# Optimization experiments

Hardware: AMD Instinct MI355X
Metric: run time of the kernel (lower is better)

Reference implementation:

```python
import jax, jax.numpy as jnp
import numpy as np

STATE_DIM, ACTION_DIM, HIDDEN_DIM = 512, 64, 2048
INPUT_DIM = STATE_DIM + ACTION_DIM + 1  # 577
BATCH = 4096


def setup_inputs() -> dict:
    key = jax.random.key(0)
    ks = jax.random.split(key, 12)
    sc_x = 1.0 / np.sqrt(INPUT_DIM)
    sc_h = 1.0 / np.sqrt(HIDDEN_DIM)
    return {
        "s": jax.random.normal(ks[0], (BATCH, STATE_DIM), jnp.float32),
        "a_prev": jax.random.normal(ks[1], (BATCH, ACTION_DIM), jnp.float32),
        "r_prev": jax.random.normal(ks[2], (BATCH, 1), jnp.float32),
        "h": jnp.zeros((HIDDEN_DIM,), jnp.float32),
        "c": jnp.zeros((HIDDEN_DIM,), jnp.float32),
        # Fused gate weights: columns ordered [i, f, g(c-tilde), o]
        "Wx": jax.random.uniform(ks[3], (INPUT_DIM, 4 * HIDDEN_DIM), jnp.float32, -sc_x, sc_x),
        "Wh": jax.random.uniform(ks[4], (HIDDEN_DIM, 4 * HIDDEN_DIM), jnp.float32, -sc_h, sc_h),
        "bh": jax.random.uniform(ks[5], (4 * HIDDEN_DIM,), jnp.float32, -sc_h, sc_h),
        "Wa": jax.random.uniform(ks[6], (HIDDEN_DIM, ACTION_DIM), jnp.float32, -sc_h, sc_h),
        "ba": jax.random.uniform(ks[7], (ACTION_DIM,), jnp.float32, -sc_h, sc_h),
        "Wv": jax.random.uniform(ks[8], (HIDDEN_DIM, 1), jnp.float32, -sc_h, sc_h),
        "bv": jax.random.uniform(ks[9], (1,), jnp.float32, -sc_h, sc_h),
    }


def reference(s, a_prev, r_prev, h, c, Wx, Wh, bh, Wa, ba, Wv, bv):
    # x: [B, input_dim]
    x = jnp.concatenate([s, a_prev, r_prev], axis=1)
    # Two fused GEMMs replace the 8 separate small linears (same math).
    z = x @ Wx + h @ Wh + bh          # [B, 4H]
    zi, zf, zg, zo = jnp.split(z, 4, axis=-1)
    i = jax.nn.sigmoid(zi)
    f = jax.nn.sigmoid(zf)
    c_new = f * c + i * jnp.tanh(zg)  # [B, H] (c broadcast over batch)
    o = jax.nn.sigmoid(zo)
    h_new = o * jnp.tanh(c_new)       # [B, H]
    probs = jax.nn.softmax(h_new @ Wa + ba, axis=1)  # [B, A]
    v = h_new @ Wv + bv               # [B, 1]
    return (probs, v)
```

## Files before the change

kernel.cpp:

```cpp
#include <hip/hip_runtime.h>
#include <hip/hip_bf16.h>

#define BATCH   4096
#define SDIM    512
#define ADIM    64
#define IDIM    577
#define KP2     640
#define NKT     20
#define HDIM    2048
#define ZDIM    8192
#define BUFE    (128 * 32)

typedef __attribute__((ext_vector_type(8))) __bf16 bf16x8;
typedef __attribute__((ext_vector_type(4))) float  accx4;

__global__ __launch_bounds__(256) void setup_kernel(
    const float* __restrict__ s, const float* __restrict__ a_prev,
    const float* __restrict__ r_prev, const float* __restrict__ h,
    const float* __restrict__ wx, const float* __restrict__ wh,
    const float* __restrict__ wa,
    __hip_bfloat16* __restrict__ xb, __hip_bfloat16* __restrict__ wxt,
    __hip_bfloat16* __restrict__ waT, float* __restrict__ zh_w)
{
    __shared__ float stile[64 * 65];
    const int bid = blockIdx.x;
    const int t = threadIdx.x;

    if (bid < 1280) {
        const int kt2 = bid >> 7;
        const int nt  = bid & 127;
        const int c4  = t & 15;
        const int rr  = t >> 4;
#pragma unroll
        for (int i = 0; i < 4; ++i) {
            const int r = rr + i * 16;
            const int k = kt2 * 64 + r;
            float4 v = (k < IDIM)
                ? *(const float4*)(wx + (size_t)k * ZDIM + nt * 64 + c4 * 4)
                : float4{0.f, 0.f, 0.f, 0.f};
            *(float4*)(stile + r * 65 + c4 * 4) = v;
        }
        __syncthreads();
        const int ch = t & 7;
#pragma unroll
        for (int i = 0; i < 2; ++i) {
            const int nr = (t >> 3) + i * 32;
            bf16x8 w8;
#pragma unroll
            for (int j = 0; j < 8; ++j)
                w8[j] = (__bf16)stile[(ch * 8 + j) * 65 + nr];
            *(bf16x8*)(wxt + (size_t)(nt * 64 + nr) * KP2 + kt2 * 64 + ch * 8)
                = w8;
        }
    } else if (bid < 1536) {
        const int zb = bid - 1280;
        const int nb = zb & 31, ky = zb >> 5;
        const int n  = nb * 256 + t;
        const float* hp  = h + ky * 256;
        const float* whp = wh + (size_t)ky * 256 * ZDIM + n;
        float p = 0.0f;
#pragma unroll 16
        for (int kk = 0; kk < 256; ++kk)
            p = fmaf(hp[kk], whp[(size_t)kk * ZDIM], p);
        zh_w[ky * ZDIM + n] = p;
    } else if (bid < 5632) {
        const int row = bid - 1536;
        const float* srow = s + (size_t)row * SDIM;
        const float* arow = a_prev + (size_t)row * ADIM;
        __hip_bfloat16* xrow = xb + (size_t)row * KP2;
        for (int c = t; c < KP2; c += 256) {
            float v;
            if (c < SDIM)        v = srow[c];
            else if (c < 576)    v = arow[c - SDIM];
            else if (c == 576)   v = r_prev[row];
            else                 v = 0.0f;
            xrow[c] = __float2bfloat16(v);
        }
    } else {
        const int wb = bid - 5632;
        const int kt = wb >> 1, at = wb & 1;
        const int c  = t & 31, r0 = t >> 5;
#pragma unroll
        for (int i = 0; i < 4; ++i) {
            int r = r0 + i * 8;
            stile[r * 33 + c] = wa[(size_t)(kt * 32 + r) * ADIM + at * 32 + c];
        }
        __syncthreads();
#pragma unroll
        for (int i = 0; i < 4; ++i) {
            int r = r0 + i * 8;
            waT[(size_t)(at * 32 + r) * HDIM + kt * 32 + c] =
                __float2bfloat16(stile[c * 33 + r]);
        }
    }
}

__global__ __launch_bounds__(256) void zh_reduce(
    const float* __restrict__ zh_w, const float* __restrict__ bh,
    float* __restrict__ zh)
{
    const int j = blockIdx.x * 256 + threadIdx.x;
    float v = bh[j];
#pragma unroll
    for (int p = 0; p < 8; ++p)
        v += zh_w[p * ZDIM + j];
    zh[j] = v;
}

__device__ __forceinline__ float sigmoid_f(float x) {
    return 1.0f / (1.0f + __expf(-x));
}
__device__ __forceinline__ float tanh_f(float x) {
    return 1.0f - 2.0f / (1.0f + __expf(2.0f * x));
}

__global__ __launch_bounds__(256, 3) void lstm_gemm(
    const __hip_bfloat16* __restrict__ xb,
    const __hip_bfloat16* __restrict__ wxt,
    const float* __restrict__ zh,
    const float* __restrict__ cvec,
    __hip_bfloat16* __restrict__ hout)
{
    __shared__ __bf16 smA[2 * BUFE];
    __shared__ __bf16 smB[2 * BUFE];
    const int t    = threadIdx.x;
    const int lane = t & 63;
    const int wid  = t >> 6;
    const int m0   = blockIdx.x * 128;
    const int n0   = blockIdx.y * 32;
    const int wm   = wid >> 1, wn = wid & 1;
    const int fl15 = lane & 15;
    const int fhi  = lane >> 4;

    accx4 acc[4][4] = {};

    const int cch = (lane & 3) ^ ((lane >> 2) & 3) ^ ((lane >> 4) & 3);
    const __bf16* gA[2]; const __bf16* gB[2]; int lofs[2];
#pragma unroll
    for (int i = 0; i < 2; ++i) {
        const int rbase = wid * 32 + i * 16;
        const int r = rbase + (lane >> 2);
        gA[i] = (const __bf16*)xb + (size_t)(m0 + r) * KP2 + cch * 8;
        const int g = r >> 5, nn = r & 31;
        gB[i] = (const __bf16*)wxt +
                (size_t)(g * HDIM + n0 + nn) * KP2 + cch * 8;
        lofs[i] = rbase * 32;
    }

    auto stage = [&](int tile, int p) {
        const int ko = tile * 32;
        const int po = p * BUFE;
#pragma unroll
        for (int i = 0; i < 2; ++i) {
            __builtin_amdgcn_global_load_lds(
                (const __attribute__((address_space(1))) void*)(gA[i] + ko),
                (__attribute__((address_space(3))) void*)(smA + po + lofs[i]),
                16, 0, 0);
            __builtin_amdgcn_global_load_lds(
                (const __attribute__((address_space(1))) void*)(gB[i] + ko),
                (__attribute__((address_space(3))) void*)(smB + po + lofs[i]),
                16, 0, 0);
        }
    };

    const int sl = ((fhi ^ (fl15 & 3) ^ ((fl15 >> 2) & 3)) * 8);

    auto compute = [&](int p) {
        const int po = p * BUFE;
        bf16x8 af[4], bfr[4];
#pragma unroll
        for (int rt = 0; rt < 4; ++rt)
            af[rt] = *(const bf16x8*)(smA + po +
                (wm * 64 + rt * 16 + fl15) * 32 + sl);
#pragma unroll
        for (int g = 0; g < 4; ++g)
            bfr[g] = *(const bf16x8*)(smB + po +
                (g * 32 + wn * 16 + fl15) * 32 + sl);
#pragma unroll
        for (int g = 0; g < 4; ++g)
#pragma unroll
            for (int rt = 0; rt < 4; ++rt)
                acc[g][rt] = __builtin_amdgcn_mfma_f32_16x16x32_bf16(
                    af[rt], bfr[g], acc[g][rt], 0, 0, 0);
    };

    stage(0, 0);
    __syncthreads();
#pragma unroll
    for (int kt = 0; kt < NKT - 1; ++kt) {
        stage(kt + 1, (kt + 1) & 1);
        compute(kt & 1);
        __syncthreads();
    }
    compute((NKT - 1) & 1);

    const int colg = n0 + wn * 16 + fl15;
    const float zhi = zh[colg];
    const float zhf = zh[HDIM + colg];
    const float zhg = zh[2 * HDIM + colg];
    const float zho = zh[3 * HDIM + colg];
    const float cv  = cvec[colg];
#pragma unroll
    for (int rt = 0; rt < 4; ++rt) {
#pragma unroll
        for (int r = 0; r < 4; ++r) {
            const int row = m0 + wm * 64 + rt * 16 + (fhi << 2) + r;
            const float zi = acc[0][rt][r] + zhi;
            const float zf = acc[1][rt][r] + zhf;
            const float zg = acc[2][rt][r] + zhg;
            const float zo = acc[3][rt][r] + zho;
            const float cn = sigmoid_f(zf) * cv + sigmoid_f(zi) * tanh_f(zg);
            const float hn = sigmoid_f(zo) * tanh_f(cn);
            hout[(size_t)row * HDIM + colg] = __float2bfloat16(hn);
        }
    }
}

__global__ __launch_bounds__(512) void head_kernel(
    const __hip_bfloat16* __restrict__ hnew,
    const __hip_bfloat16* __restrict__ waT,
    const float* __restrict__ wv,
    const float* __restrict__ ba, const float* __restrict__ bv,
    float* __restrict__ probs, float* __restrict__ vout)
{
    __shared__ float lg[2][16][68];
    __shared__ float vpart[2][16];
    const int t    = threadIdx.x;
    const int lane = t & 63;
    const int wid  = t >> 6;
    const int kh   = wid >> 2;
    const int wid2 = wid & 3;
    const int r0   = blockIdx.x * 16;
    const int fl15 = lane & 15, fhi = lane >> 4;

    const __bf16* arow = (const __bf16*)hnew +
        (size_t)(r0 + fl15) * HDIM + kh * 1024 + fhi * 8;
    const __bf16* brow = (const __bf16*)waT +
        (size_t)(wid2 * 16 + fl15) * HDIM + kh * 1024 + fhi * 8;
    const float* wvp = wv + kh * 1024 + fhi * 8;
    const bool do_v = (wid2 == 0);

    accx4 acc0 = {}, acc1 = {};
    float va0 = 0.f, va1 = 0.f, va2 = 0.f, va3 = 0.f;
#pragma unroll 4
    for (int kk = 0; kk < 1024; kk += 64) {
        bf16x8 a0 = *(const bf16x8*)(arow + kk);
        bf16x8 b0 = *(const bf16x8*)(brow + kk);
        bf16x8 a1 = *(const bf16x8*)(arow + kk + 32);
        bf16x8 b1 = *(const bf16x8*)(brow + kk + 32);
        acc0 = __builtin_amdgcn_mfma_f32_16x16x32_bf16(a0, b0, acc0, 0, 0, 0);
        acc1 = __builtin_amdgcn_mfma_f32_16x16x32_bf16(a1, b1, acc1, 0, 0, 0);
        if (do_v) {
#pragma unroll
            for (int j = 0; j < 8; j += 4) {
                va0 = fmaf((float)a0[j],     wvp[kk + j],          va0);
                va1 = fmaf((float)a0[j + 1], wvp[kk + j + 1],      va1);
                va2 = fmaf((float)a0[j + 2], wvp[kk + j + 2],      va2);
                va3 = fmaf((float)a0[j + 3], wvp[kk + j + 3],      va3);
                va0 = fmaf((float)a1[j],     wvp[kk + 32 + j],     va0);
                va1 = fmaf((float)a1[j + 1], wvp[kk + 32 + j + 1], va1);
                va2 = fmaf((float)a1[j + 2], wvp[kk + 32 + j + 2], va2);
                va3 = fmaf((float)a1[j + 3], wvp[kk + 32 + j + 3], va3);
            }
        }
    }
#pragma unroll
    for (int r = 0; r < 4; ++r)
        lg[kh][fhi * 4 + r][wid2 * 16 + fl15] = acc0[r] + acc1[r];
    if (do_v) {
        float vacc = (va0 + va1) + (va2 + va3);
        vacc += __shfl_xor(vacc, 16);
        vacc += __shfl_xor(vacc, 32);
        if (lane < 16) vpart[kh][lane] = vacc;
    }
    __syncthreads();

    const float bav = ba[lane];
#pragma unroll
    for (int i = 0; i < 2; ++i) {
        const int row = wid * 2 + i;
        const float logit = lg[0][row][lane] + lg[1][row][lane] + bav;
        float m = logit;
#pragma unroll
        for (int mask = 32; mask >= 1; mask >>= 1)
            m = fmaxf(m, __shfl_xor(m, mask));
        const float e = __expf(logit - m);
        float ssum = e;
#pragma unroll
        for (int mask = 32; mask >= 1; mask >>= 1)
            ssum += __shfl_xor(ssum, mask);
        probs[(size_t)(r0 + row) * 64 + lane] = e / ssum;
    }
    if (t < 16) vout[r0 + t] = vpart[0][t] + vpart[1][t] + bv[0];
}

extern "C" void kernel_launch(void* const* d_in, const int* in_sizes, int n_in,
                              void* d_out, int out_size, void* d_ws,
                              size_t ws_size, hipStream_t stream)
{
    const float* s      = (const float*)d_in[0];
    const float* a_prev = (const float*)d_in[1];
    const float* r_prev = (const float*)d_in[2];
    const float* h      = (const float*)d_in[3];
    const float* c      = (const float*)d_in[4];
    const float* Wx     = (const float*)d_in[5];
    const float* Wh     = (const float*)d_in[6];
    const float* bh     = (const float*)d_in[7];
    const float* Wa     = (const float*)d_in[8];
    const float* ba     = (const float*)d_in[9];
    const float* Wv     = (const float*)d_in[10];
    const float* bv     = (const float*)d_in[11];

    float* out   = (float*)d_out;
    float* probs = out;
    float* vout  = out + (size_t)BATCH * ADIM;

    char* ws = (char*)d_ws;
    __hip_bfloat16* xb   = (__hip_bfloat16*)ws;
    __hip_bfloat16* wxt  = (__hip_bfloat16*)(ws + 5242880);
    __hip_bfloat16* waT  = (__hip_bfloat16*)(ws + 15728640);
    float* zh_w          = (float*)(ws + 15990784);
    float* zh            = (float*)(ws + 16252928);
    __hip_bfloat16* hnew = (__hip_bfloat16*)(ws + 16285696);

    setup_kernel<<<5760, 256, 0, stream>>>(
        s, a_prev, r_prev, h, Wx, Wh, Wa, xb, wxt, waT, zh_w);
    zh_reduce<<<ZDIM / 256, 256, 0, stream>>>(zh_w, bh, zh);
    lstm_gemm<<<dim3(BATCH / 128, HDIM / 32), 256, 0, stream>>>(
        xb, wxt, zh, c, hnew);
    head_kernel<<<BATCH / 16, 512, 0, stream>>>(
        hnew, waT, Wv, ba, bv, probs, vout);
}
```

Baseline: 220.7 us.

## Widen LSTM GEMM K-tile to 64 and split head kernel K across eight waves

The gate GEMM now stages 64-wide K tiles with a new 8-way XOR swizzle, so the K loop has 10 iterations and half as many barriers. The larger LDS buffers lead to occupancy being lowered from 3 to 2 blocks per SIMD. The head kernel now gives each of its 8 waves a 256-wide K slice, covering all four action tiles and the value dot product, with one A fragment reused across four MFMAs. Partial results are then reduced through shared memory. The cost is less latency hiding in the GEMM and more shared-memory reduction work in the head.

```diff
diff --git a/kernel.cpp b/kernel.cpp
--- a/kernel.cpp
+++ b/kernel.cpp
@@ -6,10 +6,10 @@
 #define ADIM    64
 #define IDIM    577
 #define KP2     640
-#define NKT     20
+#define NKT64   10
 #define HDIM    2048
 #define ZDIM    8192
-#define BUFE    (128 * 32)
+#define BUFE    (128 * 64)
 
 typedef __attribute__((ext_vector_type(8))) __bf16 bf16x8;
 typedef __attribute__((ext_vector_type(4))) float  accx4;
@@ -114,7 +114,7 @@
     return 1.0f - 2.0f / (1.0f + __expf(2.0f * x));
 }
 
-__global__ __launch_bounds__(256, 3) void lstm_gemm(
+__global__ __launch_bounds__(256, 2) void lstm_gemm(
     const __hip_bfloat16* __restrict__ xb,
     const __hip_bfloat16* __restrict__ wxt,
     const float* __restrict__ zh,
@@ -134,24 +134,25 @@
 
     accx4 acc[4][4] = {};
 
-    const int cch = (lane & 3) ^ ((lane >> 2) & 3) ^ ((lane >> 4) & 3);
-    const __bf16* gA[2]; const __bf16* gB[2]; int lofs[2];
-#pragma unroll
-    for (int i = 0; i < 2; ++i) {
-        const int rbase = wid * 32 + i * 16;
-        const int r = rbase + (lane >> 2);
+    const int srow = lane >> 3;
+    const int slot = lane & 7;
+    const int cch  = slot ^ srow;
+    const __bf16* gA[4]; const __bf16* gB[4]; int lofs[4];
+#pragma unroll
+    for (int i = 0; i < 4; ++i) {
+        const int r = wid * 32 + i * 8 + srow;
         gA[i] = (const __bf16*)xb + (size_t)(m0 + r) * KP2 + cch * 8;
         const int g = r >> 5, nn = r & 31;
         gB[i] = (const __bf16*)wxt +
                 (size_t)(g * HDIM + n0 + nn) * KP2 + cch * 8;
-        lofs[i] = rbase * 32;
+        lofs[i] = (wid * 32 + i * 8) * 64;
     }
 
     auto stage = [&](int tile, int p) {
-        const int ko = tile * 32;
+        const int ko = tile * 64;
         const int po = p * BUFE;
 #pragma unroll
-        for (int i = 0; i < 2; ++i) {
+        for (int i = 0; i < 4; ++i) {
             __builtin_amdgcn_global_load_lds(
                 (const __attribute__((address_space(1))) void*)(gA[i] + ko),
                 (__attribute__((address_space(3))) void*)(smA + po + lofs[i]),
@@ -163,36 +164,39 @@
         }
     };
 
-    const int sl = ((fhi ^ (fl15 & 3) ^ ((fl15 >> 2) & 3)) * 8);
-
     auto compute = [&](int p) {
         const int po = p * BUFE;
-        bf16x8 af[4], bfr[4];
-#pragma unroll
-        for (int rt = 0; rt < 4; ++rt)
-            af[rt] = *(const bf16x8*)(smA + po +
-                (wm * 64 + rt * 16 + fl15) * 32 + sl);
-#pragma unroll
-        for (int g = 0; g < 4; ++g)
-            bfr[g] = *(const bf16x8*)(smB + po +
-                (g * 32 + wn * 16 + fl15) * 32 + sl);
-#pragma unroll
-        for (int g = 0; g < 4; ++g)
+#pragma unroll
+        for (int hf = 0; hf < 2; ++hf) {
+            const int ck = hf * 4 + fhi;
+            const int sl = (ck ^ (fl15 & 7)) * 8;
+            bf16x8 af[4], bfr[4];
 #pragma unroll
             for (int rt = 0; rt < 4; ++rt)
-                acc[g][rt] = __builtin_amdgcn_mfma_f32_16x16x32_bf16(
-                    af[rt], bfr[g], acc[g][rt], 0, 0, 0);
+                af[rt] = *(const bf16x8*)(smA + po +
+                    (wm * 64 + rt * 16 + fl15) * 64 + sl);
+#pragma unroll
+            for (int g = 0; g < 4; ++g)
+                bfr[g] = *(const bf16x8*)(smB + po +
+                    (g * 32 + wn * 16 + fl15) * 64 + sl);
+#pragma unroll
+            for (int g = 0; g < 4; ++g)
+#pragma unroll
+                for (int rt = 0; rt < 4; ++rt)
+                    acc[g][rt] = __builtin_amdgcn_mfma_f32_16x16x32_bf16(
+                        af[rt], bfr[g], acc[g][rt], 0, 0, 0);
+        }
     };
 
     stage(0, 0);
     __syncthreads();
 #pragma unroll
-    for (int kt = 0; kt < NKT - 1; ++kt) {
+    for (int kt = 0; kt < NKT64 - 1; ++kt) {
         stage(kt + 1, (kt + 1) & 1);
         compute(kt & 1);
         __syncthreads();
     }
-    compute((NKT - 1) & 1);
+    compute((NKT64 - 1) & 1);
 
     const int colg = n0 + wn * 16 + fl15;
     const float zhi = zh[colg];
@@ -223,63 +227,57 @@
     const float* __restrict__ ba, const float* __restrict__ bv,
     float* __restrict__ probs, float* __restrict__ vout)
 {
-    __shared__ float lg[2][16][68];
-    __shared__ float vpart[2][16];
+    __shared__ float lg[8][16][68];
+    __shared__ float vpart[8][16];
     const int t    = threadIdx.x;
     const int lane = t & 63;
-    const int wid  = t >> 6;
-    const int kh   = wid >> 2;
-    const int wid2 = wid & 3;
+    const int w    = t >> 6;
     const int r0   = blockIdx.x * 16;
     const int fl15 = lane & 15, fhi = lane >> 4;
+    const int k0   = w * 256;
 
     const __bf16* arow = (const __bf16*)hnew +
-        (size_t)(r0 + fl15) * HDIM + kh * 1024 + fhi * 8;
+        (size_t)(r0 + fl15) * HDIM + k0 + fhi * 8;
     const __bf16* brow = (const __bf16*)waT +
-        (size_t)(wid2 * 16 + fl15) * HDIM + kh * 1024 + fhi * 8;
-    const float* wvp = wv + kh * 1024 + fhi * 8;
-    const bool do_v = (wid2 == 0);
-
-    accx4 acc0 = {}, acc1 = {};
-    float va0 = 0.f, va1 = 0.f, va2 = 0.f, va3 = 0.f;
-#pragma unroll 4
-    for (int kk = 0; kk < 1024; kk += 64) {
-        bf16x8 a0 = *(const bf16x8*)(arow + kk);
-        bf16x8 b0 = *(const bf16x8*)(brow + kk);
-        bf16x8 a1 = *(const bf16x8*)(arow + kk + 32);
-        bf16x8 b1 = *(const bf16x8*)(brow + kk + 32);
-        acc0 = __builtin_amdgcn_mfma_f32_16x16x32_bf16(a0, b0, acc0, 0, 0, 0);
-        acc1 = __builtin_amdgcn_mfma_f32_16x16x32_bf16(a1, b1, acc1, 0, 0, 0);
-        if (do_v) {
-#pragma unroll
-            for (int j = 0; j < 8; j += 4) {
-                va0 = fmaf((float)a0[j],     wvp[kk + j],          va0);
-                va1 = fmaf((float)a0[j + 1], wvp[kk + j + 1],      va1);
-                va2 = fmaf((float)a0[j + 2], wvp[kk + j + 2],      va2);
-                va3 = fmaf((float)a0[j + 3], wvp[kk + j + 3],      va3);
-                va0 = fmaf((float)a1[j],     wvp[kk + 32 + j],     va0);
-                va1 = fmaf((float)a1[j + 1], wvp[kk + 32 + j + 1], va1);
-                va2 = fmaf((float)a1[j + 2], wvp[kk + 32 + j + 2], va2);
-                va3 = fmaf((float)a1[j + 3], wvp[kk + 32 + j + 3], va3);
-            }
-        }
-    }
-#pragma unroll
-    for (int r = 0; r < 4; ++r)
-        lg[kh][fhi * 4 + r][wid2 * 16 + fl15] = acc0[r] + acc1[r];
-    if (do_v) {
-        float vacc = (va0 + va1) + (va2 + va3);
-        vacc += __shfl_xor(vacc, 16);
-        vacc += __shfl_xor(vacc, 32);
-        if (lane < 16) vpart[kh][lane] = vacc;
-    }
+        (size_t)fl15 * HDIM + k0 + fhi * 8;
+    const float* wvp = wv + k0 + fhi * 8;
+
+    accx4 acc[4] = {};
+    float va0 = 0.f, va1 = 0.f;
+#pragma unroll
+    for (int kk = 0; kk < 256; kk += 32) {
+        bf16x8 af = *(const bf16x8*)(arow + kk);
+#pragma unroll
+        for (int a = 0; a < 4; ++a) {
+            bf16x8 bf = *(const bf16x8*)(brow + (size_t)a * 16 * HDIM + kk);
+            acc[a] = __builtin_amdgcn_mfma_f32_16x16x32_bf16(
+                af, bf, acc[a], 0, 0, 0);
+        }
+#pragma unroll
+        for (int j = 0; j < 4; ++j) {
+            va0 = fmaf((float)af[j],     wvp[kk + j],     va0);
+            va1 = fmaf((float)af[j + 4], wvp[kk + j + 4], va1);
+        }
+    }
+#pragma unroll
+    for (int a = 0; a < 4; ++a)
+#pragma unroll
+        for (int r = 0; r < 4; ++r)
+            lg[w][fhi * 4 + r][a * 16 + fl15] = acc[a][r];
+    float va = va0 + va1;
+    va += __shfl_xor(va, 16);
+    va += __shfl_xor(va, 32);
+    if (lane < 16) vpart[w][lane] = va;
     __syncthreads();
 
     const float bav = ba[lane];
 #pragma unroll
     for (int i = 0; i < 2; ++i) {
-        const int row = wid * 2 + i;
-        const float logit = lg[0][row][lane] + lg[1][row][lane] + bav;
+        const int row = w * 2 + i;
+        float logit = bav;
+#pragma unroll
+        for (int p = 0; p < 8; ++p)
+            logit += lg[p][row][lane];
         float m = logit;
 #pragma unroll
         for (int mask = 32; mask >= 1; mask >>= 1)
@@ -291,7 +289,13 @@
             ssum += __shfl_xor(ssum, mask);
         probs[(size_t)(r0 + row) * 64 + lane] = e / ssum;
     }
-    if (t < 16) vout[r0 + t] = vpart[0][t] + vpart[1][t] + bv[0];
+    if (t < 16) {
+        float v = bv[0];
+#pragma unroll
+        for (int p = 0; p < 8; ++p)
+            v += vpart[p][t];
+        vout[r0 + t] = v;
+    }
 }
 
 extern "C" void kernel_launch(void* const* d_in, const int* in_sizes, int n_in,
```

After: 213.2 us. 3.4% less time.
